# Kernel tuning notes

Measured on AMD Instinct MI355X. Metric: run time of the kernel, lower is better.

Reference implementation:

```python
import jax, jax.numpy as jnp
import numpy as np

N = 50000   # nodes
E = 800000  # edges (avg degree 16)
F = 128     # node_features


def setup_inputs() -> dict:
    key = jax.random.key(0)
    ks = jax.random.split(key, 10)
    s = 1.0 / np.sqrt(F)
    x = jax.random.normal(ks[0], (N, F), jnp.float32)
    edge_index = jax.random.randint(ks[1], (2, E), 0, N, dtype=jnp.int32)
    edge_weight = jax.random.uniform(ks[2], (E,), jnp.float32)
    # EvolveGCNO initial weight (glorot-ish) and GRU parameters (PyTorch layout)
    W0 = jax.random.uniform(ks[3], (F, F), jnp.float32, -s, s)
    W_ih = jax.random.uniform(ks[4], (3 * F, F), jnp.float32, -s, s)
    W_hh = jax.random.uniform(ks[5], (3 * F, F), jnp.float32, -s, s)
    b_ih = jax.random.uniform(ks[6], (3 * F,), jnp.float32, -s, s)
    b_hh = jax.random.uniform(ks[7], (3 * F,), jnp.float32, -s, s)
    # Linear(F, 1) head
    w_lin = jax.random.uniform(ks[8], (1, F), jnp.float32, -s, s)
    b_lin = jax.random.uniform(ks[9], (1,), jnp.float32, -s, s)
    return dict(x=x, edge_index=edge_index, edge_weight=edge_weight, W0=W0,
                W_ih=W_ih, W_hh=W_hh, b_ih=b_ih, b_hh=b_hh,
                w_lin=w_lin, b_lin=b_lin)


def _gru_evolve(W0, W_ih, W_hh, b_ih, b_hh):
    # GRU(input=W0, hidden=W0): seq_len=1, batch=F, feature=F (PyTorch gate order r,z,n)
    gi = W0 @ W_ih.T + b_ih  # [F, 3F]
    gh = W0 @ W_hh.T + b_hh  # [F, 3F]
    f = W0.shape[1]
    i_r, i_z, i_n = gi[:, :f], gi[:, f:2 * f], gi[:, 2 * f:]
    h_r, h_z, h_n = gh[:, :f], gh[:, f:2 * f], gh[:, 2 * f:]
    r = jax.nn.sigmoid(i_r + h_r)
    z = jax.nn.sigmoid(i_z + h_z)
    n = jnp.tanh(i_n + r * h_n)
    return (1.0 - z) * n + z * W0  # evolved weight [F, F]


def reference(x, edge_index, edge_weight, W0, W_ih, W_hh, b_ih, b_hh, w_lin, b_lin):
    n_nodes = x.shape[0]
    W = _gru_evolve(W0, W_ih, W_hh, b_ih, b_hh)
    # gcn_norm: add self loops (weight 1), symmetric D^-1/2 A D^-1/2
    loop = jnp.arange(n_nodes, dtype=edge_index.dtype)
    src = jnp.concatenate([edge_index[0], loop])
    dst = jnp.concatenate([edge_index[1], loop])
    w = jnp.concatenate([edge_weight, jnp.ones((n_nodes,), x.dtype)])
    deg = jax.ops.segment_sum(w, dst, num_segments=n_nodes)
    dinv = jnp.where(deg > 0, jax.lax.rsqrt(deg), 0.0)
    norm = dinv[src] * w * dinv[dst]  # [E+N]
    xw = x @ W  # [N, F]
    h = jax.ops.segment_sum(norm[:, None] * xw[src], dst, num_segments=n_nodes)
    h = jnp.tanh(h)
    return h @ w_lin.T + b_lin  # [N, 1]
```

## Files before the change

### kernel.cpp

```cpp
#include <hip/hip_runtime.h>
#include <hip/hip_bf16.h>
#include <math.h>

#define N_NODES 50000
#define N_EDGES 800000
#define FDIM 128
#define SCAN_BLOCKS 196

typedef unsigned int uint32;
typedef __attribute__((ext_vector_type(8))) __bf16 bf16x8;
typedef __attribute__((ext_vector_type(8))) short short8;
typedef __attribute__((ext_vector_type(16))) float f32x16;

__device__ inline unsigned short f2bf(float f) {
  unsigned int u = __float_as_uint(f);
  unsigned int r = u + 0x7fffu + ((u >> 16) & 1u);
  return (unsigned short)(r >> 16);
}

__global__ __launch_bounds__(384) void evolve_kernel(
    const float* __restrict__ W0, const float* __restrict__ Wih,
    const float* __restrict__ Whh, const float* __restrict__ bih,
    const float* __restrict__ bhh, float* __restrict__ W) {
  int i = blockIdx.x;
  int jj = threadIdx.x;
  __shared__ float w0s[FDIM];
  __shared__ float gis[3 * FDIM];
  __shared__ float ghs[3 * FDIM];
  if (jj < FDIM) w0s[jj] = W0[i * FDIM + jj];
  __syncthreads();
  float gi = bih[jj], gh = bhh[jj];
  const float4* wih4 = (const float4*)(Wih + jj * FDIM);
  const float4* whh4 = (const float4*)(Whh + jj * FDIM);
#pragma unroll 8
  for (int k = 0; k < FDIM / 4; k++) {
    float4 a = wih4[k];
    float4 b = whh4[k];
    float w0a = w0s[4 * k], w0b = w0s[4 * k + 1];
    float w0c = w0s[4 * k + 2], w0d = w0s[4 * k + 3];
    gi += a.x * w0a + a.y * w0b + a.z * w0c + a.w * w0d;
    gh += b.x * w0a + b.y * w0b + b.z * w0c + b.w * w0d;
  }
  gis[jj] = gi;
  ghs[jj] = gh;
  __syncthreads();
  if (jj < FDIM) {
    float r = 1.0f / (1.0f + expf(-(gis[jj] + ghs[jj])));
    float z = 1.0f / (1.0f + expf(-(gis[jj + FDIM] + ghs[jj + FDIM])));
    float nn = tanhf(gis[jj + 2 * FDIM] + r * ghs[jj + 2 * FDIM]);
    W[i * FDIM + jj] = (1.0f - z) * nn + z * w0s[jj];
  }
}

__global__ void hist_kernel(const int* __restrict__ ei, int* __restrict__ cnt,
                            int* __restrict__ rank, int e) {
  int idx = blockIdx.x * blockDim.x + threadIdx.x;
  if (idx < e) {
    int dst = ei[N_EDGES + idx];
    rank[idx] = atomicAdd(&cnt[dst], 1);
  }
}

__global__ __launch_bounds__(256) void partial_kernel(
    const int* __restrict__ cnt, int* __restrict__ part, int n) {
  int t = threadIdx.x;
  int idx = blockIdx.x * 256 + t;
  int v = (idx < n) ? cnt[idx] : 0;
  int r = v;
#pragma unroll
  for (int o = 32; o > 0; o >>= 1) r += __shfl_down(r, o, 64);
  __shared__ int s[4];
  if ((t & 63) == 0) s[t >> 6] = r;
  __syncthreads();
  if (t == 0) part[blockIdx.x] = s[0] + s[1] + s[2] + s[3];
}

__global__ __launch_bounds__(256) void scan_part_kernel(int* __restrict__ part) {
  __shared__ int tmp[256];
  int t = threadIdx.x;
  int v = (t < SCAN_BLOCKS) ? part[t] : 0;
  tmp[t] = v;
  __syncthreads();
#pragma unroll
  for (int off = 1; off < 256; off <<= 1) {
    int u = (t >= off) ? tmp[t - off] : 0;
    __syncthreads();
    tmp[t] += u;
    __syncthreads();
  }
  if (t < SCAN_BLOCKS) part[t] = tmp[t] - v;
}

__global__ __launch_bounds__(256) void scan_final_kernel(
    const int* __restrict__ cnt, const int* __restrict__ part,
    int* __restrict__ offs, int n) {
  __shared__ int tmp[256];
  int t = threadIdx.x;
  int idx = blockIdx.x * 256 + t;
  int v = (idx < n) ? cnt[idx] : 0;
  tmp[t] = v;
  __syncthreads();
#pragma unroll
  for (int off = 1; off < 256; off <<= 1) {
    int u = (t >= off) ? tmp[t - off] : 0;
    __syncthreads();
    tmp[t] += u;
    __syncthreads();
  }
  int excl = part[blockIdx.x] + tmp[t] - v;
  if (idx < n) offs[idx] = excl;
  if (idx == n - 1) offs[n] = excl + v;
}

__global__ void scatter_kernel(const int* __restrict__ ei,
                               const float* __restrict__ ew,
                               const int* __restrict__ offs,
                               const int* __restrict__ rank,
                               int2* __restrict__ csr, int e) {
  int idx = blockIdx.x * blockDim.x + threadIdx.x;
  if (idx < e) {
    int src = ei[idx];
    int dst = ei[N_EDGES + idx];
    int pos = offs[dst] + rank[idx];
    csr[pos] = make_int2(src, __float_as_int(ew[idx]));
  }
}

__global__ __launch_bounds__(256) void deg_dinv_kernel(
    const int2* __restrict__ csr, const int* __restrict__ offs,
    float* __restrict__ dinv, int n) {
  int i = blockIdx.x * blockDim.x + threadIdx.x;
  if (i >= n) return;
  int b = offs[i], e = offs[i + 1];
  float d = 1.0f;
  for (int j = b; j < e; j++) d += __int_as_float(csr[j].y);
  dinv[i] = (d > 0.0f) ? rsqrtf(d) : 0.0f;
}

__global__ __launch_bounds__(256) void xw_mfma_kernel(
    const float* __restrict__ x, const float* __restrict__ W,
    const float* __restrict__ dinv, unsigned short* __restrict__ y, int n) {
  __shared__ short Bs[16 * 128 * 8];
  int t = threadIdx.x;
#pragma unroll
  for (int i = 0; i < 64; i++) {
    int idx = i * 256 + t;
    int k = idx >> 7, nn = idx & 127;
    Bs[(((k >> 3) << 7) + nn) * 8 + (k & 7)] = (short)f2bf(W[idx]);
  }
  __syncthreads();

  int lane = t & 63;
  int wid = blockIdx.x * 4 + (t >> 6);
  int tr = wid * 32;
  if (tr >= n) return;
  int m = lane & 31;
  int q2 = lane >> 5;

  int row = tr + m;
  if (row >= n) row = n - 1;
  const float* xr = x + (size_t)row * FDIM;

  bf16x8 a[8];
#pragma unroll
  for (int kc = 0; kc < 8; kc++) {
    int k0 = kc * 16 + q2 * 8;
    float4 p = *(const float4*)(xr + k0);
    float4 q = *(const float4*)(xr + k0 + 4);
    short8 s;
    s[0] = (short)f2bf(p.x); s[1] = (short)f2bf(p.y);
    s[2] = (short)f2bf(p.z); s[3] = (short)f2bf(p.w);
    s[4] = (short)f2bf(q.x); s[5] = (short)f2bf(q.y);
    s[6] = (short)f2bf(q.z); s[7] = (short)f2bf(q.w);
    a[kc] = __builtin_bit_cast(bf16x8, s);
  }

  f32x16 acc[4];
#pragma unroll
  for (int ct = 0; ct < 4; ct++) {
#pragma unroll
    for (int r = 0; r < 16; r++) acc[ct][r] = 0.0f;
  }
#pragma unroll
  for (int ct = 0; ct < 4; ct++) {
    int nn = ct * 32 + m;
#pragma unroll
    for (int kc = 0; kc < 8; kc++) {
      int kg = kc * 2 + q2;
      bf16x8 b = __builtin_bit_cast(
          bf16x8, *(const short8*)(Bs + (((kg << 7) + nn) << 3)));
      acc[ct] = __builtin_amdgcn_mfma_f32_32x32x16_bf16(a[kc], b, acc[ct], 0,
                                                        0, 0);
    }
  }

#pragma unroll
  for (int r = 0; r < 16; r++) {
    int rl = (r & 3) + ((r >> 2) << 3) + (q2 << 2);
    int rg = tr + rl;
    if (rg < n) {
      float dv = dinv[rg];
#pragma unroll
      for (int ct = 0; ct < 4; ct++) {
        y[(size_t)rg * FDIM + ct * 32 + m] = f2bf(dv * acc[ct][r]);
      }
    }
  }
}

__global__ __launch_bounds__(256) void gather_kernel(
    const uint32* __restrict__ yb, const int* __restrict__ offs,
    const int2* __restrict__ csr, const float* __restrict__ dinv,
    const float* __restrict__ wl, const float* __restrict__ bl,
    float* __restrict__ out, int n) {
  int wid = (int)((blockIdx.x * (size_t)blockDim.x + threadIdx.x) >> 6);
  int lane = threadIdx.x & 63;
  if (wid >= n) return;
  float di = dinv[wid];
  uint32 uv = yb[(size_t)wid * 64 + lane];
  float ax = __uint_as_float(uv << 16);
  float ay = __uint_as_float(uv & 0xffff0000u);
  int beg = offs[wid], end = offs[wid + 1];
  int e = beg;
  for (; e + 4 <= end; e += 4) {
    int2 c0 = csr[e];
    int2 c1 = csr[e + 1];
    int2 c2 = csr[e + 2];
    int2 c3 = csr[e + 3];
    uint32 u0 = yb[(size_t)c0.x * 64 + lane];
    uint32 u1 = yb[(size_t)c1.x * 64 + lane];
    uint32 u2 = yb[(size_t)c2.x * 64 + lane];
    uint32 u3 = yb[(size_t)c3.x * 64 + lane];
    float w0 = __int_as_float(c0.y), w1 = __int_as_float(c1.y);
    float w2 = __int_as_float(c2.y), w3 = __int_as_float(c3.y);
    ax += w0 * __uint_as_float(u0 << 16);
    ay += w0 * __uint_as_float(u0 & 0xffff0000u);
    ax += w1 * __uint_as_float(u1 << 16);
    ay += w1 * __uint_as_float(u1 & 0xffff0000u);
    ax += w2 * __uint_as_float(u2 << 16);
    ay += w2 * __uint_as_float(u2 & 0xffff0000u);
    ax += w3 * __uint_as_float(u3 << 16);
    ay += w3 * __uint_as_float(u3 & 0xffff0000u);
  }
  for (; e < end; e++) {
    int2 c = csr[e];
    uint32 u = yb[(size_t)c.x * 64 + lane];
    float wn = __int_as_float(c.y);
    ax += wn * __uint_as_float(u << 16);
    ay += wn * __uint_as_float(u & 0xffff0000u);
  }
  float2 wv = ((const float2*)wl)[lane];
  float p = tanhf(di * ax) * wv.x + tanhf(di * ay) * wv.y;
#pragma unroll
  for (int o = 32; o > 0; o >>= 1) p += __shfl_down(p, o, 64);
  if (lane == 0) out[wid] = p + bl[0];
}

extern "C" void kernel_launch(void* const* d_in, const int* in_sizes, int n_in,
                              void* d_out, int out_size, void* d_ws,
                              size_t ws_size, hipStream_t stream) {
  const float* x = (const float*)d_in[0];
  const int* ei = (const int*)d_in[1];
  const float* ew = (const float*)d_in[2];
  const float* W0 = (const float*)d_in[3];
  const float* Wih = (const float*)d_in[4];
  const float* Whh = (const float*)d_in[5];
  const float* bih = (const float*)d_in[6];
  const float* bhh = (const float*)d_in[7];
  const float* wl = (const float*)d_in[8];
  const float* bl = (const float*)d_in[9];
  float* out = (float*)d_out;

  float* ws = (float*)d_ws;
  float* W_ev = ws;
  unsigned short* y = (unsigned short*)(W_ev + 16384);
  float* dinv = (float*)(y + (size_t)N_NODES * FDIM);
  int* cnt = (int*)(dinv + N_NODES);
  int* rank = cnt + N_NODES;
  int* offs = rank + N_EDGES;
  int2* csr = (int2*)(offs + 50004);
  int* part = (int*)(csr + N_EDGES);

  evolve_kernel<<<FDIM, 384, 0, stream>>>(W0, Wih, Whh, bih, bhh, W_ev);
  hipMemsetAsync(cnt, 0, sizeof(int) * N_NODES, stream);
  hist_kernel<<<(N_EDGES + 255) / 256, 256, 0, stream>>>(ei, cnt, rank,
                                                         N_EDGES);
  partial_kernel<<<SCAN_BLOCKS, 256, 0, stream>>>(cnt, part, N_NODES);
  scan_part_kernel<<<1, 256, 0, stream>>>(part);
  scan_final_kernel<<<SCAN_BLOCKS, 256, 0, stream>>>(cnt, part, offs, N_NODES);
  scatter_kernel<<<(N_EDGES + 255) / 256, 256, 0, stream>>>(ei, ew, offs, rank,
                                                            csr, N_EDGES);
  deg_dinv_kernel<<<(N_NODES + 255) / 256, 256, 0, stream>>>(csr, offs, dinv,
                                                             N_NODES);
  xw_mfma_kernel<<<391, 256, 0, stream>>>(x, W_ev, dinv, y, N_NODES);
  gather_kernel<<<(N_NODES * 64) / 256, 256, 0, stream>>>(
      (const uint32*)y, offs, csr, dinv, wl, bl, out, N_NODES);
}
```

Before: 214.2 us.

## Fuse histogram with XW matmul, single-pass scan, move dinv scaling into gather

Zeroes the count array inside the evolve kernel instead of a separate memset. Merges the edge histogram and the XW MFMA matmul into one launch with disjoint block roles, so XW no longer waits on the degree computation. Replaces the three scan kernels with one kernel that hands block partial sums across blocks through global flags and spin-waits, assuming all 196 blocks are resident at once. Since y is no longer scaled by the source dinv, the gather loads dinv per neighbour, adding a random read for each edge in exchange for fewer launches and less serialisation.

Result: no change. 212.3 us (-0.9%).

```diff
diff --git a/kernel.cpp b/kernel.cpp
--- a/kernel.cpp
+++ b/kernel.cpp
@@ -6,12 +6,17 @@
 #define N_EDGES 800000
 #define FDIM 128
 #define SCAN_BLOCKS 196
+#define XW_BLOCKS 391
 
 typedef unsigned int uint32;
 typedef __attribute__((ext_vector_type(8))) __bf16 bf16x8;
 typedef __attribute__((ext_vector_type(8))) short short8;
 typedef __attribute__((ext_vector_type(16))) float f32x16;
 
+#define FLAG_A 200
+#define FLAG_B 201
+#define SCANNED 256
+
 __device__ inline unsigned short f2bf(float f) {
   unsigned int u = __float_as_uint(f);
   unsigned int r = u + 0x7fffu + ((u >> 16) & 1u);
@@ -21,9 +26,15 @@
 __global__ __launch_bounds__(384) void evolve_kernel(
     const float* __restrict__ W0, const float* __restrict__ Wih,
     const float* __restrict__ Whh, const float* __restrict__ bih,
-    const float* __restrict__ bhh, float* __restrict__ W) {
+    const float* __restrict__ bhh, float* __restrict__ W,
+    int* __restrict__ cnt, int* __restrict__ part) {
   int i = blockIdx.x;
   int jj = threadIdx.x;
+  int gid = i * 384 + jj;
+  for (int j = gid; j < N_NODES; j += 128 * 384) cnt[j] = 0;
+  if (gid == 0) part[FLAG_A] = 0;
+  if (gid == 1) part[FLAG_B] = 0;
+
   __shared__ float w0s[FDIM];
   __shared__ float gis[3 * FDIM];
   __shared__ float ghs[3 * FDIM];
@@ -52,33 +63,93 @@
   }
 }
 
-__global__ void hist_kernel(const int* __restrict__ ei, int* __restrict__ cnt,
-                            int* __restrict__ rank, int e) {
-  int idx = blockIdx.x * blockDim.x + threadIdx.x;
-  if (idx < e) {
-    int dst = ei[N_EDGES + idx];
-    rank[idx] = atomicAdd(&cnt[dst], 1);
-  }
-}
-
-__global__ __launch_bounds__(256) void partial_kernel(
-    const int* __restrict__ cnt, int* __restrict__ part, int n) {
+__global__ __launch_bounds__(256) void histxw_kernel(
+    const int* __restrict__ ei, int* __restrict__ cnt, int* __restrict__ rank,
+    const float* __restrict__ x, const float* __restrict__ W,
+    unsigned short* __restrict__ y, int n) {
+  __shared__ short Bs[16 * 128 * 8];
   int t = threadIdx.x;
-  int idx = blockIdx.x * 256 + t;
-  int v = (idx < n) ? cnt[idx] : 0;
-  int r = v;
-#pragma unroll
-  for (int o = 32; o > 0; o >>= 1) r += __shfl_down(r, o, 64);
-  __shared__ int s[4];
-  if ((t & 63) == 0) s[t >> 6] = r;
-  __syncthreads();
-  if (t == 0) part[blockIdx.x] = s[0] + s[1] + s[2] + s[3];
-}
-
-__global__ __launch_bounds__(256) void scan_part_kernel(int* __restrict__ part) {
+  if (blockIdx.x >= XW_BLOCKS) {
+    int idx = (blockIdx.x - XW_BLOCKS) * 256 + t;
+    if (idx < N_EDGES) {
+      int dst = ei[N_EDGES + idx];
+      rank[idx] = atomicAdd(&cnt[dst], 1);
+    }
+    return;
+  }
+#pragma unroll
+  for (int i = 0; i < 64; i++) {
+    int idx = i * 256 + t;
+    int k = idx >> 7, nn = idx & 127;
+    Bs[(((k >> 3) << 7) + nn) * 8 + (k & 7)] = (short)f2bf(W[idx]);
+  }
+  __syncthreads();
+
+  int lane = t & 63;
+  int wid = blockIdx.x * 4 + (t >> 6);
+  int tr = wid * 32;
+  if (tr >= n) return;
+  int m = lane & 31;
+  int q2 = lane >> 5;
+
+  int row = tr + m;
+  if (row >= n) row = n - 1;
+  const float* xr = x + (size_t)row * FDIM;
+
+  bf16x8 a[8];
+#pragma unroll
+  for (int kc = 0; kc < 8; kc++) {
+    int k0 = kc * 16 + q2 * 8;
+    float4 p = *(const float4*)(xr + k0);
+    float4 q = *(const float4*)(xr + k0 + 4);
+    short8 s;
+    s[0] = (short)f2bf(p.x); s[1] = (short)f2bf(p.y);
+    s[2] = (short)f2bf(p.z); s[3] = (short)f2bf(p.w);
+    s[4] = (short)f2bf(q.x); s[5] = (short)f2bf(q.y);
+    s[6] = (short)f2bf(q.z); s[7] = (short)f2bf(q.w);
+    a[kc] = __builtin_bit_cast(bf16x8, s);
+  }
+
+  f32x16 acc[4];
+#pragma unroll
+  for (int ct = 0; ct < 4; ct++) {
+#pragma unroll
+    for (int r = 0; r < 16; r++) acc[ct][r] = 0.0f;
+  }
+#pragma unroll
+  for (int ct = 0; ct < 4; ct++) {
+    int nn = ct * 32 + m;
+#pragma unroll
+    for (int kc = 0; kc < 8; kc++) {
+      int kg = kc * 2 + q2;
+      bf16x8 b = __builtin_bit_cast(
+          bf16x8, *(const short8*)(Bs + (((kg << 7) + nn) << 3)));
+      acc[ct] = __builtin_amdgcn_mfma_f32_32x32x16_bf16(a[kc], b, acc[ct], 0,
+                                                        0, 0);
+    }
+  }
+
+#pragma unroll
+  for (int r = 0; r < 16; r++) {
+    int rl = (r & 3) + ((r >> 2) << 3) + (q2 << 2);
+    int rg = tr + rl;
+    if (rg < n) {
+#pragma unroll
+      for (int ct = 0; ct < 4; ct++) {
+        y[(size_t)rg * FDIM + ct * 32 + m] = f2bf(acc[ct][r]);
+      }
+    }
+  }
+}
+
+__global__ __launch_bounds__(256) void scan_all_kernel(
+    const int* __restrict__ cnt, int* __restrict__ part, int* __restrict__ offs,
+    int n) {
   __shared__ int tmp[256];
   int t = threadIdx.x;
-  int v = (t < SCAN_BLOCKS) ? part[t] : 0;
+  int bid = blockIdx.x;
+  int idx = bid * 256 + t;
+  int v = (idx < n) ? cnt[idx] : 0;
   tmp[t] = v;
   __syncthreads();
 #pragma unroll
@@ -88,26 +159,54 @@
     tmp[t] += u;
     __syncthreads();
   }
-  if (t < SCAN_BLOCKS) part[t] = tmp[t] - v;
-}
-
-__global__ __launch_bounds__(256) void scan_final_kernel(
-    const int* __restrict__ cnt, const int* __restrict__ part,
-    int* __restrict__ offs, int n) {
-  __shared__ int tmp[256];
-  int t = threadIdx.x;
-  int idx = blockIdx.x * 256 + t;
-  int v = (idx < n) ? cnt[idx] : 0;
-  tmp[t] = v;
-  __syncthreads();
-#pragma unroll
-  for (int off = 1; off < 256; off <<= 1) {
-    int u = (t >= off) ? tmp[t - off] : 0;
-    __syncthreads();
-    tmp[t] += u;
-    __syncthreads();
-  }
-  int excl = part[blockIdx.x] + tmp[t] - v;
+  int local_excl = tmp[t] - v;
+  int block_sum = tmp[255];
+  if (t == 0) {
+    __hip_atomic_store(&part[bid], block_sum, __ATOMIC_RELEASE,
+                       __HIP_MEMORY_SCOPE_AGENT);
+    __hip_atomic_fetch_add(&part[FLAG_A], 1, __ATOMIC_ACQ_REL,
+                           __HIP_MEMORY_SCOPE_AGENT);
+  }
+  if (bid == 0) {
+    if (t == 0) {
+      while (__hip_atomic_load(&part[FLAG_A], __ATOMIC_ACQUIRE,
+                               __HIP_MEMORY_SCOPE_AGENT) < SCAN_BLOCKS) {
+        __builtin_amdgcn_s_sleep(1);
+      }
+    }
+    __syncthreads();
+    __shared__ int ps[256];
+    int pv = (t < SCAN_BLOCKS)
+                 ? __hip_atomic_load(&part[t], __ATOMIC_RELAXED,
+                                     __HIP_MEMORY_SCOPE_AGENT)
+                 : 0;
+    ps[t] = pv;
+    __syncthreads();
+#pragma unroll
+    for (int off = 1; off < 256; off <<= 1) {
+      int u = (t >= off) ? ps[t - off] : 0;
+      __syncthreads();
+      ps[t] += u;
+      __syncthreads();
+    }
+    if (t < SCAN_BLOCKS)
+      __hip_atomic_store(&part[SCANNED + t], ps[t] - pv, __ATOMIC_RELAXED,
+                         __HIP_MEMORY_SCOPE_AGENT);
+    __syncthreads();
+    if (t == 0)
+      __hip_atomic_store(&part[FLAG_B], 1, __ATOMIC_RELEASE,
+                         __HIP_MEMORY_SCOPE_AGENT);
+  }
+  if (t == 0) {
+    while (__hip_atomic_load(&part[FLAG_B], __ATOMIC_ACQUIRE,
+                             __HIP_MEMORY_SCOPE_AGENT) == 0) {
+      __builtin_amdgcn_s_sleep(1);
+    }
+  }
+  __syncthreads();
+  int base = __hip_atomic_load(&part[SCANNED + bid], __ATOMIC_RELAXED,
+                               __HIP_MEMORY_SCOPE_AGENT);
+  int excl = base + local_excl;
   if (idx < n) offs[idx] = excl;
   if (idx == n - 1) offs[n] = excl + v;
 }
@@ -137,77 +236,6 @@
   dinv[i] = (d > 0.0f) ? rsqrtf(d) : 0.0f;
 }
 
-__global__ __launch_bounds__(256) void xw_mfma_kernel(
-    const float* __restrict__ x, const float* __restrict__ W,
-    const float* __restrict__ dinv, unsigned short* __restrict__ y, int n) {
-  __shared__ short Bs[16 * 128 * 8];
-  int t = threadIdx.x;
-#pragma unroll
-  for (int i = 0; i < 64; i++) {
-    int idx = i * 256 + t;
-    int k = idx >> 7, nn = idx & 127;
-    Bs[(((k >> 3) << 7) + nn) * 8 + (k & 7)] = (short)f2bf(W[idx]);
-  }
-  __syncthreads();
-
-  int lane = t & 63;
-  int wid = blockIdx.x * 4 + (t >> 6);
-  int tr = wid * 32;
-  if (tr >= n) return;
-  int m = lane & 31;
-  int q2 = lane >> 5;
-
-  int row = tr + m;
-  if (row >= n) row = n - 1;
-  const float* xr = x + (size_t)row * FDIM;
-
-  bf16x8 a[8];
-#pragma unroll
-  for (int kc = 0; kc < 8; kc++) {
-    int k0 = kc * 16 + q2 * 8;
-    float4 p = *(const float4*)(xr + k0);
-    float4 q = *(const float4*)(xr + k0 + 4);
-    short8 s;
-    s[0] = (short)f2bf(p.x); s[1] = (short)f2bf(p.y);
-    s[2] = (short)f2bf(p.z); s[3] = (short)f2bf(p.w);
-    s[4] = (short)f2bf(q.x); s[5] = (short)f2bf(q.y);
-    s[6] = (short)f2bf(q.z); s[7] = (short)f2bf(q.w);
-    a[kc] = __builtin_bit_cast(bf16x8, s);
-  }
-
-  f32x16 acc[4];
-#pragma unroll
-  for (int ct = 0; ct < 4; ct++) {
-#pragma unroll
-    for (int r = 0; r < 16; r++) acc[ct][r] = 0.0f;
-  }
-#pragma unroll
-  for (int ct = 0; ct < 4; ct++) {
-    int nn = ct * 32 + m;
-#pragma unroll
-    for (int kc = 0; kc < 8; kc++) {
-      int kg = kc * 2 + q2;
-      bf16x8 b = __builtin_bit_cast(
-          bf16x8, *(const short8*)(Bs + (((kg << 7) + nn) << 3)));
-      acc[ct] = __builtin_amdgcn_mfma_f32_32x32x16_bf16(a[kc], b, acc[ct], 0,
-                                                        0, 0);
-    }
-  }
-
-#pragma unroll
-  for (int r = 0; r < 16; r++) {
-    int rl = (r & 3) + ((r >> 2) << 3) + (q2 << 2);
-    int rg = tr + rl;
-    if (rg < n) {
-      float dv = dinv[rg];
-#pragma unroll
-      for (int ct = 0; ct < 4; ct++) {
-        y[(size_t)rg * FDIM + ct * 32 + m] = f2bf(dv * acc[ct][r]);
-      }
-    }
-  }
-}
-
 __global__ __launch_bounds__(256) void gather_kernel(
     const uint32* __restrict__ yb, const int* __restrict__ offs,
     const int2* __restrict__ csr, const float* __restrict__ dinv,
@@ -218,8 +246,8 @@
   if (wid >= n) return;
   float di = dinv[wid];
   uint32 uv = yb[(size_t)wid * 64 + lane];
-  float ax = __uint_as_float(uv << 16);
-  float ay = __uint_as_float(uv & 0xffff0000u);
+  float ax = di * __uint_as_float(uv << 16);
+  float ay = di * __uint_as_float(uv & 0xffff0000u);
   int beg = offs[wid], end = offs[wid + 1];
   int e = beg;
   for (; e + 4 <= end; e += 4) {
@@ -231,8 +259,10 @@
     uint32 u1 = yb[(size_t)c1.x * 64 + lane];
     uint32 u2 = yb[(size_t)c2.x * 64 + lane];
     uint32 u3 = yb[(size_t)c3.x * 64 + lane];
-    float w0 = __int_as_float(c0.y), w1 = __int_as_float(c1.y);
-    float w2 = __int_as_float(c2.y), w3 = __int_as_float(c3.y);
+    float w0 = __int_as_float(c0.y) * dinv[c0.x];
+    float w1 = __int_as_float(c1.y) * dinv[c1.x];
+    float w2 = __int_as_float(c2.y) * dinv[c2.x];
+    float w3 = __int_as_float(c3.y) * dinv[c3.x];
     ax += w0 * __uint_as_float(u0 << 16);
     ay += w0 * __uint_as_float(u0 & 0xffff0000u);
     ax += w1 * __uint_as_float(u1 << 16);
@@ -245,7 +275,7 @@
   for (; e < end; e++) {
     int2 c = csr[e];
     uint32 u = yb[(size_t)c.x * 64 + lane];
-    float wn = __int_as_float(c.y);
+    float wn = __int_as_float(c.y) * dinv[c.x];
     ax += wn * __uint_as_float(u << 16);
     ay += wn * __uint_as_float(u & 0xffff0000u);
   }
@@ -281,18 +311,15 @@
   int2* csr = (int2*)(offs + 50004);
   int* part = (int*)(csr + N_EDGES);
 
-  evolve_kernel<<<FDIM, 384, 0, stream>>>(W0, Wih, Whh, bih, bhh, W_ev);
-  hipMemsetAsync(cnt, 0, sizeof(int) * N_NODES, stream);
-  hist_kernel<<<(N_EDGES + 255) / 256, 256, 0, stream>>>(ei, cnt, rank,
-                                                         N_EDGES);
-  partial_kernel<<<SCAN_BLOCKS, 256, 0, stream>>>(cnt, part, N_NODES);
-  scan_part_kernel<<<1, 256, 0, stream>>>(part);
-  scan_final_kernel<<<SCAN_BLOCKS, 256, 0, stream>>>(cnt, part, offs, N_NODES);
+  evolve_kernel<<<FDIM, 384, 0, stream>>>(W0, Wih, Whh, bih, bhh, W_ev, cnt,
+                                          part);
+  histxw_kernel<<<XW_BLOCKS + (N_EDGES + 255) / 256, 256, 0, stream>>>(
+      ei, cnt, rank, x, W_ev, y, N_NODES);
+  scan_all_kernel<<<SCAN_BLOCKS, 256, 0, stream>>>(cnt, part, offs, N_NODES);
   scatter_kernel<<<(N_EDGES + 255) / 256, 256, 0, stream>>>(ei, ew, offs, rank,
                                                             csr, N_EDGES);
   deg_dinv_kernel<<<(N_NODES + 255) / 256, 256, 0, stream>>>(csr, offs, dinv,
                                                              N_NODES);
-  xw_mfma_kernel<<<391, 256, 0, stream>>>(x, W_ev, dinv, y, N_NODES);
   gather_kernel<<<(N_NODES * 64) / 256, 256, 0, stream>>>(
       (const uint32*)y, offs, csr, dinv, wl, bl, out, N_NODES);
 }
```
